# Performance work log

Measured on AMD Instinct MI355X. Metric: run time of the kernel, lower is better.

## Reference

```python
import jax, jax.numpy as jnp
import numpy as np

CODE_STD = 0.01
EPS = 1e-12


def setup_inputs() -> dict:
    key = jax.random.key(0)
    kx, kc = jax.random.split(key)
    N, D, K = 8192, 512, 16384
    x = jax.random.normal(kx, (N, D), dtype=jnp.float32)
    codebook = CODE_STD * jax.random.normal(kc, (K, D), dtype=jnp.float32)
    return {"x": x, "codebook": codebook}


def reference(x, codebook):
    # normalize_embedding: L2-normalize each embedding vector
    emb = x / jnp.maximum(jnp.linalg.norm(x, axis=-1, keepdims=True), EPS)
    # [N, D] @ [D, K] -> [N, K] similarities
    sims = emb @ codebook.T
    best = jnp.argmax(sims, axis=1)            # [N] int32
    return codebook[best]                       # [N, D] gathered codes
```

## Files before the change

### kernel.cpp

```cpp
#include <hip/hip_runtime.h>
#include <hip/hip_bf16.h>
#include <stdint.h>


typedef _Float16 half8 __attribute__((ext_vector_type(8)));
typedef _Float16 half4v __attribute__((ext_vector_type(4)));
typedef float f32x4 __attribute__((ext_vector_type(4)));

#define M_ROWS 8192
#define DIM 512
#define K_CODES 16384
#define BM 128
#define BN 128
#define BK 32
#define NSPLIT 32
#define NT ((K_CODES / NSPLIT) / BN)
#define NEG_INF (-3.402823466e+38f)
#define MARGIN 2.0e-3f

typedef __attribute__((address_space(1))) uint32_t as1_u32;
typedef __attribute__((address_space(3))) uint32_t as3_u32;

__device__ __forceinline__ void gll16(const void* g, void* l) {
  __builtin_amdgcn_global_load_lds((const as1_u32*)(uintptr_t)g,
                                   (as3_u32*)(uintptr_t)l, 16, 0, 0);
}

__device__ __forceinline__ void stage_tile(const _Float16* __restrict__ g_base,
                                           _Float16* lds_tile, int tid) {
#pragma unroll
  for (int r = 0; r < 2; ++r) {
    const int s = r * 256 + tid;
    const int row = s >> 2;
    const int kc = (s & 3) ^ ((row >> 1) & 3);
    const _Float16* g = g_base + (size_t)row * DIM + (kc << 3);
    _Float16* l = lds_tile + ((size_t)(r * 256 + (tid & 192)) << 3);
    gll16((const void*)g, (void*)l);
  }
}

__global__ void to_f16(const float* __restrict__ src, _Float16* __restrict__ dst, int n4) {
  int i = blockIdx.x * 256 + threadIdx.x;
  if (i >= n4) return;
  const float4 v = reinterpret_cast<const float4*>(src)[i];
  half4v h = {(_Float16)v.x, (_Float16)v.y, (_Float16)v.z, (_Float16)v.w};
  reinterpret_cast<half4v*>(dst)[i] = h;
}

__global__ __launch_bounds__(256, 2) void vq_argmax(
    const _Float16* __restrict__ xh, const _Float16* __restrict__ ch,
    float* __restrict__ pv, int* __restrict__ pi) {
  __shared__ _Float16 sxh[BM * BK];
  __shared__ _Float16 sch[BN * BK];
  __shared__ float rv1[2][BM], rv2[2][BM];
  __shared__ int ri1[2][BM], ri2[2][BM];

  const int tid = threadIdx.x;
  const int w = tid >> 6, lane = tid & 63;
  const int wm = w & 1, wn = w >> 1;
  const int l15 = lane & 15, quad = lane >> 4;
  const int row0 = blockIdx.x * BM;
  const int split = blockIdx.y;
  const int n_base = split * (K_CODES / NSPLIT);
  const int kq = ((quad ^ ((l15 >> 1) & 3)) << 3);

  float bv1[4][4], bv2[4][4];
  int bi1[4][4], bi2[4][4];
#pragma unroll
  for (int i = 0; i < 4; ++i)
#pragma unroll
    for (int r = 0; r < 4; ++r) {
      bv1[i][r] = NEG_INF; bv2[i][r] = NEG_INF;
      bi1[i][r] = 0x7fffffff; bi2[i][r] = 0x7fffffff;
    }

#pragma unroll 1
  for (int nt = 0; nt < NT; ++nt) {
    const int n0 = n_base + nt * BN;
    f32x4 acc[4][4];
#pragma unroll
    for (int i = 0; i < 4; ++i)
#pragma unroll
      for (int j = 0; j < 4; ++j) acc[i][j] = (f32x4){0.f, 0.f, 0.f, 0.f};

#pragma unroll 1
    for (int ks = 0; ks < DIM / BK; ++ks) {
      const int k0 = ks * BK;
      stage_tile(xh + (size_t)row0 * DIM + k0, sxh, tid);
      stage_tile(ch + (size_t)n0 * DIM + k0, sch, tid);
      __syncthreads();

      half8 A[4], B[4];
#pragma unroll
      for (int i = 0; i < 4; ++i) {
        A[i] = *(const half8*)&sxh[(wm * 64 + i * 16 + l15) * BK + kq];
        B[i] = *(const half8*)&sch[(wn * 64 + i * 16 + l15) * BK + kq];
      }
#pragma unroll
      for (int i = 0; i < 4; ++i)
#pragma unroll
        for (int j = 0; j < 4; ++j)
          acc[i][j] = __builtin_amdgcn_mfma_f32_16x16x32_f16(A[i], B[j], acc[i][j], 0, 0, 0);
      __syncthreads();
    }

#pragma unroll
    for (int i = 0; i < 4; ++i)
#pragma unroll
      for (int r = 0; r < 4; ++r)
#pragma unroll
        for (int j = 0; j < 4; ++j) {
          float s = acc[i][j][r];
          int c = n0 + wn * 64 + j * 16 + l15;
          if (s > bv1[i][r]) {
            bv2[i][r] = bv1[i][r]; bi2[i][r] = bi1[i][r];
            bv1[i][r] = s; bi1[i][r] = c;
          } else if (s > bv2[i][r]) {
            bv2[i][r] = s; bi2[i][r] = c;
          }
        }
  }

#pragma unroll
  for (int i = 0; i < 4; ++i)
#pragma unroll
    for (int r = 0; r < 4; ++r) {
      float a1 = bv1[i][r], a2 = bv2[i][r];
      int x1 = bi1[i][r], x2 = bi2[i][r];
#pragma unroll
      for (int d = 1; d < 16; d <<= 1) {
        float b1 = __shfl_xor(a1, d), b2 = __shfl_xor(a2, d);
        int y1 = __shfl_xor(x1, d), y2 = __shfl_xor(x2, d);
        bool bw = (b1 > a1) || (b1 == a1 && y1 < x1);
        float w1 = bw ? b1 : a1;  int wi = bw ? y1 : x1;
        float l1 = bw ? a1 : b1;  int li = bw ? x1 : y1;
        float s2 = bw ? b2 : a2;  int si = bw ? y2 : x2;
        bool t = (s2 > l1) || (s2 == l1 && si < li);
        a1 = w1; x1 = wi;
        a2 = t ? s2 : l1; x2 = t ? si : li;
      }
      bv1[i][r] = a1; bi1[i][r] = x1; bv2[i][r] = a2; bi2[i][r] = x2;
    }

  if (l15 == 0) {
#pragma unroll
    for (int i = 0; i < 4; ++i)
#pragma unroll
      for (int r = 0; r < 4; ++r) {
        const int rl = wm * 64 + i * 16 + quad * 4 + r;
        rv1[wn][rl] = bv1[i][r]; ri1[wn][rl] = bi1[i][r];
        rv2[wn][rl] = bv2[i][r]; ri2[wn][rl] = bi2[i][r];
      }
  }
  __syncthreads();
  if (tid < BM) {
    float a1 = rv1[0][tid], a2 = rv2[0][tid];
    int x1 = ri1[0][tid], x2 = ri2[0][tid];
    float b1 = rv1[1][tid], b2 = rv2[1][tid];
    int y1 = ri1[1][tid], y2 = ri2[1][tid];
    bool bw = (b1 > a1) || (b1 == a1 && y1 < x1);
    float w1 = bw ? b1 : a1;  int wi = bw ? y1 : x1;
    float l1 = bw ? a1 : b1;  int li = bw ? x1 : y1;
    float s2 = bw ? b2 : a2;  int si = bw ? y2 : x2;
    bool t = (s2 > l1) || (s2 == l1 && si < li);
    float m2 = t ? s2 : l1;  int mi2 = t ? si : li;
    const size_t o = (size_t)(row0 + tid) * (NSPLIT * 2) + split * 2;
    pv[o] = w1; pi[o] = wi;
    pv[o + 1] = m2; pi[o + 1] = mi2;
  }
}

__global__ void recheck_gather(const float* __restrict__ pv, const int* __restrict__ pi,
                               const float* __restrict__ x, const float* __restrict__ cb,
                               float* __restrict__ out) {
  const int row = blockIdx.x;
  const int lane = threadIdx.x;
  float v = pv[(size_t)row * 64 + lane];
  int ci = pi[(size_t)row * 64 + lane];

  float m1 = v; int mi1 = ci;
#pragma unroll
  for (int d = 1; d < 64; d <<= 1) {
    float ov = __shfl_xor(m1, d);
    int oi = __shfl_xor(mi1, d);
    if (ov > m1 || (ov == m1 && oi < mi1)) { m1 = ov; mi1 = oi; }
  }

  const bool flag = (v >= m1 - MARGIN);
  const unsigned long long mask = __ballot(flag);
  int winner;
  if (__popcll(mask) == 1) {
    winner = mi1;
  } else {
    double e = -1.0e300;
    if (flag) {
      const float* xr = x + (size_t)row * DIM;
      const float* cr = cb + (size_t)ci * DIM;
      double s = 0.0;
#pragma unroll 4
      for (int t = 0; t < DIM; t += 4) {
        const float4 a = *(const float4*)(xr + t);
        const float4 b = *(const float4*)(cr + t);
        s += (double)a.x * b.x + (double)a.y * b.y + (double)a.z * b.z + (double)a.w * b.w;
      }
      e = s;
    }
    int ei = flag ? ci : 0x7fffffff;
#pragma unroll
    for (int d = 1; d < 64; d <<= 1) {
      double oe = __shfl_xor(e, d);
      int oi = __shfl_xor(ei, d);
      if (oe > e || (oe == e && oi < ei)) { e = oe; ei = oi; }
    }
    winner = ei;
  }

  const float4* src = (const float4*)(cb + (size_t)winner * DIM);
  float4* dst = (float4*)(out + (size_t)row * DIM);
  dst[lane] = src[lane];
  dst[lane + 64] = src[lane + 64];
}

extern "C" void kernel_launch(void* const* d_in, const int* in_sizes, int n_in,
                              void* d_out, int out_size, void* d_ws, size_t ws_size,
                              hipStream_t stream) {
  const float* x = (const float*)d_in[0];
  const float* cb = (const float*)d_in[1];
  float* out = (float*)d_out;

  _Float16* xh = (_Float16*)d_ws;
  _Float16* ch = xh + (size_t)M_ROWS * DIM;
  float* pv = (float*)(ch + (size_t)K_CODES * DIM);
  int* pi = (int*)(pv + (size_t)M_ROWS * NSPLIT * 2);

  to_f16<<<(M_ROWS * DIM / 4) / 256, 256, 0, stream>>>(x, xh, M_ROWS * DIM / 4);
  to_f16<<<(K_CODES * DIM / 4) / 256, 256, 0, stream>>>(cb, ch, K_CODES * DIM / 4);
  vq_argmax<<<dim3(M_ROWS / BM, NSPLIT), 256, 0, stream>>>(xh, ch, pv, pi);
  recheck_gather<<<M_ROWS, 64, 0, stream>>>(pv, pi, x, cb, out);
}
```

Before: 311.8 us.

## Switch similarity GEMM to FP8 MFMA with codebook scaling and wider recheck margin

Converts x and a scaled codebook to FP8 in one fused conversion kernel. The argmax GEMM then runs on the MX-scaled 16x16x128 f8f6f4 MFMA with a BK=128 swizzled LDS layout, which halves operand bytes and increases matrix throughput. NSPLIT is doubled so the recheck now takes 128 candidates per row. The margin is widened to absorb FP8 error, and an exact double-precision recheck resolves near ties. The cost is more candidates needing the fp64 dot-product recheck, and a risk of mis-selection if FP8 error ever exceeds the margin.

```diff
diff --git a/kernel.cpp b/kernel.cpp
--- a/kernel.cpp
+++ b/kernel.cpp
@@ -3,20 +3,23 @@
 #include <stdint.h>
 
 
-typedef _Float16 half8 __attribute__((ext_vector_type(8)));
-typedef _Float16 half4v __attribute__((ext_vector_type(4)));
 typedef float f32x4 __attribute__((ext_vector_type(4)));
+typedef int int4v __attribute__((ext_vector_type(4)));
+typedef int int8v __attribute__((ext_vector_type(8)));
 
 #define M_ROWS 8192
 #define DIM 512
 #define K_CODES 16384
 #define BM 128
 #define BN 128
-#define BK 32
-#define NSPLIT 32
+#define BK 128
+#define NSPLIT 64
 #define NT ((K_CODES / NSPLIT) / BN)
 #define NEG_INF (-3.402823466e+38f)
-#define MARGIN 2.0e-3f
+#define MARGIN 3.2f
+#define CB_SCALE 64.0f
+#define N4X (M_ROWS * DIM / 4)
+#define N4C (K_CODES * DIM / 4)
 
 typedef __attribute__((address_space(1))) uint32_t as1_u32;
 typedef __attribute__((address_space(3))) uint32_t as3_u32;
@@ -26,32 +29,43 @@
                                    (as3_u32*)(uintptr_t)l, 16, 0, 0);
 }
 
-__device__ __forceinline__ void stage_tile(const _Float16* __restrict__ g_base,
-                                           _Float16* lds_tile, int tid) {
-#pragma unroll
-  for (int r = 0; r < 2; ++r) {
+__device__ __forceinline__ void stage_tile_fp8(const uint8_t* __restrict__ g_base,
+                                               uint8_t* lds_tile, int tid) {
+#pragma unroll
+  for (int r = 0; r < 4; ++r) {
     const int s = r * 256 + tid;
-    const int row = s >> 2;
-    const int kc = (s & 3) ^ ((row >> 1) & 3);
-    const _Float16* g = g_base + (size_t)row * DIM + (kc << 3);
-    _Float16* l = lds_tile + ((size_t)(r * 256 + (tid & 192)) << 3);
+    const int row = s >> 3;
+    const int kc = (s & 7) ^ (row & 7);
+    const uint8_t* g = g_base + (size_t)row * DIM + (kc << 4);
+    uint8_t* l = lds_tile + ((size_t)(r * 256 + (tid & 192)) << 4);
     gll16((const void*)g, (void*)l);
   }
 }
 
-__global__ void to_f16(const float* __restrict__ src, _Float16* __restrict__ dst, int n4) {
+__global__ void cvt_fp8(const float* __restrict__ x, const float* __restrict__ cb,
+                        uint8_t* __restrict__ xd, uint8_t* __restrict__ cd) {
   int i = blockIdx.x * 256 + threadIdx.x;
-  if (i >= n4) return;
+  const float* src;
+  uint8_t* dst;
+  float sc;
+  if (i < N4X) {
+    src = x; dst = xd; sc = 1.0f;
+  } else {
+    src = cb; dst = cd; sc = CB_SCALE; i -= N4X;
+    if (i >= N4C) return;
+  }
   const float4 v = reinterpret_cast<const float4*>(src)[i];
-  half4v h = {(_Float16)v.x, (_Float16)v.y, (_Float16)v.z, (_Float16)v.w};
-  reinterpret_cast<half4v*>(dst)[i] = h;
+  int w = 0;
+  w = __builtin_amdgcn_cvt_pk_fp8_f32(v.x * sc, v.y * sc, w, false);
+  w = __builtin_amdgcn_cvt_pk_fp8_f32(v.z * sc, v.w * sc, w, true);
+  reinterpret_cast<int*>(dst)[i] = w;
 }
 
 __global__ __launch_bounds__(256, 2) void vq_argmax(
-    const _Float16* __restrict__ xh, const _Float16* __restrict__ ch,
+    const uint8_t* __restrict__ xq, const uint8_t* __restrict__ cq,
     float* __restrict__ pv, int* __restrict__ pi) {
-  __shared__ _Float16 sxh[BM * BK];
-  __shared__ _Float16 sch[BN * BK];
+  __shared__ __align__(16) uint8_t sxa[BM * BK];
+  __shared__ __align__(16) uint8_t scb[BN * BK];
   __shared__ float rv1[2][BM], rv2[2][BM];
   __shared__ int ri1[2][BM], ri2[2][BM];
 
@@ -62,7 +76,7 @@
   const int row0 = blockIdx.x * BM;
   const int split = blockIdx.y;
   const int n_base = split * (K_CODES / NSPLIT);
-  const int kq = ((quad ^ ((l15 >> 1) & 3)) << 3);
+  const int sw = l15 & 7;
 
   float bv1[4][4], bv2[4][4];
   int bi1[4][4], bi2[4][4];
@@ -86,21 +100,30 @@
 #pragma unroll 1
     for (int ks = 0; ks < DIM / BK; ++ks) {
       const int k0 = ks * BK;
-      stage_tile(xh + (size_t)row0 * DIM + k0, sxh, tid);
-      stage_tile(ch + (size_t)n0 * DIM + k0, sch, tid);
+      stage_tile_fp8(xq + (size_t)row0 * DIM + k0, sxa, tid);
+      stage_tile_fp8(cq + (size_t)n0 * DIM + k0, scb, tid);
       __syncthreads();
 
-      half8 A[4], B[4];
+      int8v A[4], B[4];
 #pragma unroll
       for (int i = 0; i < 4; ++i) {
-        A[i] = *(const half8*)&sxh[(wm * 64 + i * 16 + l15) * BK + kq];
-        B[i] = *(const half8*)&sch[(wn * 64 + i * 16 + l15) * BK + kq];
+        const int ra = (wm * 64 + i * 16 + l15) * BK;
+        const int rb = (wn * 64 + i * 16 + l15) * BK;
+        int4v alo = *(const int4v*)&sxa[ra + ((((quad << 1) | 0) ^ sw) << 4)];
+        int4v ahi = *(const int4v*)&sxa[ra + ((((quad << 1) | 1) ^ sw) << 4)];
+        int4v blo = *(const int4v*)&scb[rb + ((((quad << 1) | 0) ^ sw) << 4)];
+        int4v bhi = *(const int4v*)&scb[rb + ((((quad << 1) | 1) ^ sw) << 4)];
+        A[i] = __builtin_shufflevector(alo, ahi, 0, 1, 2, 3, 4, 5, 6, 7);
+        B[i] = __builtin_shufflevector(blo, bhi, 0, 1, 2, 3, 4, 5, 6, 7);
       }
 #pragma unroll
       for (int i = 0; i < 4; ++i)
 #pragma unroll
         for (int j = 0; j < 4; ++j)
-          acc[i][j] = __builtin_amdgcn_mfma_f32_16x16x32_f16(A[i], B[j], acc[i][j], 0, 0, 0);
+          acc[i][j] = __builtin_amdgcn_mfma_scale_f32_16x16x128_f8f6f4(
+              A[i], B[j], acc[i][j], 0 , 0 ,
+              0, 0x7F7F7F7F ,
+              0, 0x7F7F7F7F );
       __syncthreads();
     }
 
@@ -170,15 +193,29 @@
   }
 }
 
+__device__ double dot64(const float* __restrict__ a, const float* __restrict__ b) {
+  double s0 = 0, s1 = 0, s2 = 0, s3 = 0;
+#pragma unroll 4
+  for (int t = 0; t < DIM; t += 4) {
+    const float4 u = *(const float4*)(a + t);
+    const float4 v = *(const float4*)(b + t);
+    s0 += (double)u.x * v.x; s1 += (double)u.y * v.y;
+    s2 += (double)u.z * v.z; s3 += (double)u.w * v.w;
+  }
+  return (s0 + s1) + (s2 + s3);
+}
+
 __global__ void recheck_gather(const float* __restrict__ pv, const int* __restrict__ pi,
                                const float* __restrict__ x, const float* __restrict__ cb,
                                float* __restrict__ out) {
   const int row = blockIdx.x;
   const int lane = threadIdx.x;
-  float v = pv[(size_t)row * 64 + lane];
-  int ci = pi[(size_t)row * 64 + lane];
-
-  float m1 = v; int mi1 = ci;
+  const size_t base = (size_t)row * (NSPLIT * 2);
+  float v0 = pv[base + lane];      int c0 = pi[base + lane];
+  float v1 = pv[base + 64 + lane]; int c1 = pi[base + 64 + lane];
+
+  bool b = (v1 > v0) || (v1 == v0 && c1 < c0);
+  float m1 = b ? v1 : v0; int mi1 = b ? c1 : c0;
 #pragma unroll
   for (int d = 1; d < 64; d <<= 1) {
     float ov = __shfl_xor(m1, d);
@@ -186,26 +223,20 @@
     if (ov > m1 || (ov == m1 && oi < mi1)) { m1 = ov; mi1 = oi; }
   }
 
-  const bool flag = (v >= m1 - MARGIN);
-  const unsigned long long mask = __ballot(flag);
+  const bool f0 = (v0 >= m1 - MARGIN);
+  const bool f1 = (v1 >= m1 - MARGIN);
+  const int nf = __popcll(__ballot(f0)) + __popcll(__ballot(f1));
   int winner;
-  if (__popcll(mask) == 1) {
+  if (nf == 1) {
     winner = mi1;
   } else {
-    double e = -1.0e300;
-    if (flag) {
-      const float* xr = x + (size_t)row * DIM;
-      const float* cr = cb + (size_t)ci * DIM;
-      double s = 0.0;
-#pragma unroll 4
-      for (int t = 0; t < DIM; t += 4) {
-        const float4 a = *(const float4*)(xr + t);
-        const float4 b = *(const float4*)(cr + t);
-        s += (double)a.x * b.x + (double)a.y * b.y + (double)a.z * b.z + (double)a.w * b.w;
-      }
-      e = s;
-    }
-    int ei = flag ? ci : 0x7fffffff;
+    const float* xr = x + (size_t)row * DIM;
+    double e = -1.0e300; int ei = 0x7fffffff;
+    if (f0) { e = dot64(xr, cb + (size_t)c0 * DIM); ei = c0; }
+    if (f1) {
+      double e2 = dot64(xr, cb + (size_t)c1 * DIM);
+      if (e2 > e || (e2 == e && c1 < ei)) { e = e2; ei = c1; }
+    }
 #pragma unroll
     for (int d = 1; d < 64; d <<= 1) {
       double oe = __shfl_xor(e, d);
@@ -228,13 +259,12 @@
   const float* cb = (const float*)d_in[1];
   float* out = (float*)d_out;
 
-  _Float16* xh = (_Float16*)d_ws;
-  _Float16* ch = xh + (size_t)M_ROWS * DIM;
-  float* pv = (float*)(ch + (size_t)K_CODES * DIM);
+  uint8_t* xq = (uint8_t*)d_ws;
+  uint8_t* cq = xq + (size_t)M_ROWS * DIM;
+  float* pv = (float*)(cq + (size_t)K_CODES * DIM);
   int* pi = (int*)(pv + (size_t)M_ROWS * NSPLIT * 2);
 
-  to_f16<<<(M_ROWS * DIM / 4) / 256, 256, 0, stream>>>(x, xh, M_ROWS * DIM / 4);
-  to_f16<<<(K_CODES * DIM / 4) / 256, 256, 0, stream>>>(cb, ch, K_CODES * DIM / 4);
-  vq_argmax<<<dim3(M_ROWS / BM, NSPLIT), 256, 0, stream>>>(xh, ch, pv, pi);
+  cvt_fp8<<<(N4X + N4C + 255) / 256, 256, 0, stream>>>(x, cb, xq, cq);
+  vq_argmax<<<dim3(M_ROWS / BM, NSPLIT), 256, 0, stream>>>(xq, cq, pv, pi);
   recheck_gather<<<M_ROWS, 64, 0, stream>>>(pv, pi, x, cb, out);
 }
```

After: 321.7 us. 3.2% more time.
